# Optimization experiments

Measured on AMD Instinct MI355X. Metric: run time of the kernel, lower is better.

Reference implementation:

```python
import jax, jax.numpy as jnp
import numpy as np

N_DST = 100000


def setup_inputs() -> dict:
    key = jax.random.key(0)
    ks = jax.random.split(key, 12)
    R, Ns, E, Din, H = 3, 100000, 1000000, 128, 64
    return {
        "dst_feat": jax.random.normal(ks[0], (N_DST, Din), jnp.float32),
        "neigh_feats": jax.random.normal(ks[1], (R, Ns, Din), jnp.float32),
        "Wt": jax.random.normal(ks[2], (R + 1, Din, H), jnp.float32) * 0.05,
        "bt": jnp.zeros((R + 1, H), jnp.float32),
        "attn_l": jax.random.normal(ks[3], (R, H), jnp.float32) * 0.1,
        "attn_r": jax.random.normal(ks[4], (R, H), jnp.float32) * 0.1,
        "W1": jax.random.normal(ks[5], (H, 128), jnp.float32) * 0.1,
        "b1": jnp.zeros((128,), jnp.float32),
        "w2": jax.random.normal(ks[6], (128, 1), jnp.float32) * 0.1,
        "src_idx": jax.random.randint(ks[7], (R, E), 0, Ns, jnp.int32),
        "dst_idx": jax.random.randint(ks[8], (R, E), 0, N_DST, jnp.int32),
    }


def _gat_relation(h_src, h_dst, al, ar, src, dst):
    # el/er: per-node attention logits (dot with attn vectors)
    el = h_src @ al  # [Ns]
    er = h_dst @ ar  # [Nd]
    e = jax.nn.leaky_relu(el[src] + er[dst], 0.01)  # [E]
    # edge softmax per destination node (segment softmax)
    m = jax.ops.segment_max(e, dst, num_segments=N_DST)
    a = jnp.exp(e - m[dst])
    s = jax.ops.segment_sum(a, dst, num_segments=N_DST)
    a = a / s[dst]
    # weighted aggregation: sum_e a_e * h_src[src_e]
    out = jax.ops.segment_sum(h_src[src] * a[:, None], dst, num_segments=N_DST)
    return jax.nn.elu(out)


def reference(dst_feat, neigh_feats, Wt, bt, attn_l, attn_r, W1, b1, w2, src_idx, dst_idx):
    R = neigh_feats.shape[0]
    h_dst = dst_feat @ Wt[0] + bt[0]  # weight_T[0]
    z_r = []
    for r in range(R):
        h_src = neigh_feats[r] @ Wt[r + 1] + bt[r + 1]
        z_r.append(_gat_relation(h_src, h_dst, attn_l[r], attn_r[r], src_idx[r], dst_idx[r]))
    z_r = jnp.stack(z_r, axis=1)  # [N, R, D]
    # semantic attention
    w = (jnp.tanh(z_r @ W1 + b1) @ w2).mean(axis=0)  # [R, 1]
    a_w = jax.nn.softmax(w, axis=0)  # softmax over relations
    z = (z_r * a_w[None]).sum(axis=1)  # [N, D]
    return z
```

## Files before the change

### kernel.cpp

```cpp
#include <hip/hip_runtime.h>
#include <hip/hip_fp16.h>

#define N_DST 100000
#define DIN 128
#define HDIM 64
#define RREL 3
#define NE 1000000

#define NBKT_REL 196
#define NBKT (RREL * NBKT_REL)
#define NSEG (RREL * N_DST)
#define EDGE_CHUNK 16384
#define NBLK_BIN ((RREL * NE + EDGE_CHUNK - 1) / EDGE_CHUNK)

typedef _Float16 f16x8 __attribute__((ext_vector_type(8)));
typedef float f32x4 __attribute__((ext_vector_type(4)));

__global__ __launch_bounds__(256) void k_gemm(
    const float* __restrict__ dst_feat, const float* __restrict__ neigh,
    const float* __restrict__ Wt, const float* __restrict__ bt,
    const float* __restrict__ attn_l, const float* __restrict__ attn_r,
    __half* __restrict__ h16, float* __restrict__ el, float* __restrict__ er) {
  const int RB = (N_DST + 127) / 128;
  int mat = blockIdx.x / RB;
  int row0 = (blockIdx.x % RB) * 128;
  const float* A = (mat == 0) ? dst_feat : (neigh + (size_t)(mat - 1) * N_DST * DIN);
  const float* W = Wt + (size_t)mat * DIN * HDIM;
  const float* b = bt + mat * HDIM;

  __shared__ __align__(16) unsigned char lds[48 * 1024];
  unsigned char* ldsA = lds;
  unsigned char* ldsW = lds + 32768;

  int tid = threadIdx.x;

#pragma unroll
  for (int i = 0; i < 8; i++) {
    int s = tid + 256 * i;
    int row = s >> 4;
    int kb = s & 15;
    int gr = row0 + row;
    if (gr >= N_DST) gr = N_DST - 1;
    const float* ap = A + (size_t)gr * DIN + kb * 8;
    float4 v0 = *(const float4*)ap;
    float4 v1 = *(const float4*)(ap + 4);
    f16x8 hv;
    hv[0] = (_Float16)v0.x; hv[1] = (_Float16)v0.y;
    hv[2] = (_Float16)v0.z; hv[3] = (_Float16)v0.w;
    hv[4] = (_Float16)v1.x; hv[5] = (_Float16)v1.y;
    hv[6] = (_Float16)v1.z; hv[7] = (_Float16)v1.w;
    *(f16x8*)(ldsA + row * 256 + ((kb * 16) ^ ((row & 7) << 4))) = hv;
  }

  {
    int col = tid & 63;
    int kq = tid >> 6;
    const float* wp = W + (size_t)(kq * 32) * HDIM + col;
    float wr[32];
#pragma unroll
    for (int m = 0; m < 32; m++) wr[m] = wp[(size_t)m * HDIM];
#pragma unroll
    for (int m8 = 0; m8 < 4; m8++) {
      f16x8 hv;
#pragma unroll
      for (int j = 0; j < 8; j++) hv[j] = (_Float16)wr[m8 * 8 + j];
      int byt = kq * 64 + m8 * 16;
      *(f16x8*)(ldsW + col * 256 + (byt ^ ((col & 7) << 4))) = hv;
    }
  }
  __syncthreads();

  int w = tid >> 6;
  int l = tid & 63;
  int li = l & 15;
  int hi = l >> 4;
  f32x4 acc[2][4] = {};
#pragma unroll
  for (int ks = 0; ks < 4; ks++) {
    int kbyte = ks * 64 + hi * 16;
    f16x8 af[2], bf[4];
#pragma unroll
    for (int rt = 0; rt < 2; rt++) {
      int row = w * 32 + rt * 16 + li;
      af[rt] = *(f16x8*)(ldsA + row * 256 + (kbyte ^ ((row & 7) << 4)));
    }
#pragma unroll
    for (int ct = 0; ct < 4; ct++) {
      int col = ct * 16 + li;
      bf[ct] = *(f16x8*)(ldsW + col * 256 + (kbyte ^ ((col & 7) << 4)));
    }
#pragma unroll
    for (int rt = 0; rt < 2; rt++)
#pragma unroll
      for (int ct = 0; ct < 4; ct++)
        acc[rt][ct] = __builtin_amdgcn_mfma_f32_16x16x32_f16(af[rt], bf[ct], acc[rt][ct], 0, 0, 0);
  }

  float bv[4];
#pragma unroll
  for (int ct = 0; ct < 4; ct++) bv[ct] = b[ct * 16 + li];
#pragma unroll
  for (int rt = 0; rt < 2; rt++)
#pragma unroll
    for (int ct = 0; ct < 4; ct++)
#pragma unroll
      for (int j = 0; j < 4; j++) acc[rt][ct][j] += bv[ct];

  if (mat == 0) {
#pragma unroll
    for (int r = 0; r < RREL; r++) {
      float av[4];
#pragma unroll
      for (int ct = 0; ct < 4; ct++) av[ct] = attn_r[r * HDIM + ct * 16 + li];
#pragma unroll
      for (int rt = 0; rt < 2; rt++) {
        float p[4];
#pragma unroll
        for (int j = 0; j < 4; j++)
          p[j] = acc[rt][0][j] * av[0] + acc[rt][1][j] * av[1] +
                 acc[rt][2][j] * av[2] + acc[rt][3][j] * av[3];
#pragma unroll
        for (int o = 1; o < 16; o <<= 1)
#pragma unroll
          for (int j = 0; j < 4; j++) p[j] += __shfl_xor(p[j], o);
        if (li == 0) {
#pragma unroll
          for (int j = 0; j < 4; j++) {
            int gr = row0 + w * 32 + rt * 16 + hi * 4 + j;
            if (gr < N_DST) er[r * N_DST + gr] = p[j];
          }
        }
      }
    }
  } else {
    int r = mat - 1;
    float av[4];
#pragma unroll
    for (int ct = 0; ct < 4; ct++) av[ct] = attn_l[r * HDIM + ct * 16 + li];
#pragma unroll
    for (int rt = 0; rt < 2; rt++) {
      float p[4];
#pragma unroll
      for (int j = 0; j < 4; j++)
        p[j] = acc[rt][0][j] * av[0] + acc[rt][1][j] * av[1] +
               acc[rt][2][j] * av[2] + acc[rt][3][j] * av[3];
#pragma unroll
      for (int o = 1; o < 16; o <<= 1)
#pragma unroll
        for (int j = 0; j < 4; j++) p[j] += __shfl_xor(p[j], o);
      if (li == 0) {
#pragma unroll
        for (int j = 0; j < 4; j++) {
          int gr = row0 + w * 32 + rt * 16 + hi * 4 + j;
          if (gr < N_DST) el[r * N_DST + gr] = p[j];
        }
      }
    }
    __half* hb = h16 + (size_t)r * N_DST * HDIM;
#pragma unroll
    for (int rt = 0; rt < 2; rt++)
#pragma unroll
      for (int j = 0; j < 4; j++) {
        int gr = row0 + w * 32 + rt * 16 + hi * 4 + j;
        if (gr < N_DST) {
#pragma unroll
          for (int ct = 0; ct < 4; ct++)
            hb[(size_t)gr * HDIM + ct * 16 + li] = __float2half(acc[rt][ct][j]);
        }
      }
  }
}


__global__ __launch_bounds__(256) void k_hist(const int* __restrict__ dst_idx,
                                              int* __restrict__ hist) {
  __shared__ int h[NBKT];
  int tid = threadIdx.x;
  int blk = blockIdx.x;
  for (int i = tid; i < NBKT; i += 256) h[i] = 0;
  __syncthreads();
  int e0 = blk * EDGE_CHUNK;
  int e1 = min(e0 + EDGE_CHUNK, RREL * NE);
  for (int idx = e0 + tid; idx < e1; idx += 256) {
    int r = idx / NE;
    int d = dst_idx[idx];
    atomicAdd(&h[r * NBKT_REL + (d >> 9)], 1);
  }
  __syncthreads();
  for (int i = tid; i < NBKT; i += 256)
    hist[(size_t)i * NBLK_BIN + blk] = h[i];
}

__global__ __launch_bounds__(256) void k_colscan(int* __restrict__ hist,
                                                 int* __restrict__ bcounts) {
  __shared__ int sm[256];
  int b = blockIdx.x;
  int tid = threadIdx.x;
  int v = (tid < NBLK_BIN) ? hist[(size_t)b * NBLK_BIN + tid] : 0;
  sm[tid] = v;
  __syncthreads();
  for (int off = 1; off < 256; off <<= 1) {
    int t = (tid >= off) ? sm[tid - off] : 0;
    __syncthreads();
    sm[tid] += t;
    __syncthreads();
  }
  if (tid < NBLK_BIN) hist[(size_t)b * NBLK_BIN + tid] = sm[tid] - v;
  if (tid == 255) bcounts[b] = sm[255];
}

__global__ __launch_bounds__(256) void k_bscan(const int* __restrict__ bcounts,
                                               int* __restrict__ bucket_base,
                                               int* __restrict__ offsets) {
  __shared__ int sm[256];
  int tid = threadIdx.x;
  int base = tid * 3;
  int c[3];
#pragma unroll
  for (int k = 0; k < 3; k++) c[k] = (base + k < NBKT) ? bcounts[base + k] : 0;
  int tsum = c[0] + c[1] + c[2];
  sm[tid] = tsum;
  __syncthreads();
  for (int off = 1; off < 256; off <<= 1) {
    int v = (tid >= off) ? sm[tid - off] : 0;
    __syncthreads();
    sm[tid] += v;
    __syncthreads();
  }
  int run = sm[tid] - tsum;
#pragma unroll
  for (int k = 0; k < 3; k++) {
    if (base + k < NBKT) bucket_base[base + k] = run;
    run += c[k];
  }
  if (tid == 255) bucket_base[NBKT] = sm[255];
  if (tid == 0) offsets[NSEG] = RREL * NE;
}

__global__ __launch_bounds__(256) void k_place(const int* __restrict__ src_idx,
                                               const int* __restrict__ dst_idx,
                                               const int* __restrict__ hist,
                                               const int* __restrict__ bucket_base,
                                               unsigned* __restrict__ tmp) {
  __shared__ int cur[NBKT];
  int tid = threadIdx.x;
  int blk = blockIdx.x;
  for (int i = tid; i < NBKT; i += 256)
    cur[i] = bucket_base[i] + hist[(size_t)i * NBLK_BIN + blk];
  __syncthreads();
  int e0 = blk * EDGE_CHUNK;
  int e1 = min(e0 + EDGE_CHUNK, RREL * NE);
  for (int idx = e0 + tid; idx < e1; idx += 256) {
    int r = idx / NE;
    int d = dst_idx[idx];
    int s = src_idx[idx];
    int bucket = r * NBKT_REL + (d >> 9);
    int pos = atomicAdd(&cur[bucket], 1);
    tmp[pos] = ((unsigned)(d & 511) << 17) | (unsigned)s;
  }
}

__global__ __launch_bounds__(256) void k_bucket_csr(
    const int* __restrict__ bucket_base, const unsigned* __restrict__ tmp,
    int* __restrict__ src_sorted, int* __restrict__ offsets) {
  __shared__ int cnt[512];
  __shared__ int base_l[512];
  __shared__ int sm[256];
  int b = blockIdx.x;
  int r = b / NBKT_REL;
  int brel = b - r * NBKT_REL;
  int gbase = bucket_base[b];
  int gend = bucket_base[b + 1];
  int tid = threadIdx.x;
  cnt[tid] = 0;
  cnt[tid + 256] = 0;
  __syncthreads();
  for (int e = gbase + tid; e < gend; e += 256)
    atomicAdd(&cnt[tmp[e] >> 17], 1);
  __syncthreads();
  int c0 = cnt[2 * tid], c1 = cnt[2 * tid + 1];
  int tsum = c0 + c1;
  sm[tid] = tsum;
  __syncthreads();
  for (int off = 1; off < 256; off <<= 1) {
    int v = (tid >= off) ? sm[tid - off] : 0;
    __syncthreads();
    sm[tid] += v;
    __syncthreads();
  }
  int run = sm[tid] - tsum;
  base_l[2 * tid] = run;
  base_l[2 * tid + 1] = run + c0;
  __syncthreads();
  for (int s = tid; s < 512; s += 256) {
    int dst = (brel << 9) + s;
    if (dst < N_DST) offsets[r * N_DST + dst] = gbase + base_l[s];
    cnt[s] = 0;
  }
  __syncthreads();
  for (int e = gbase + tid; e < gend; e += 256) {
    unsigned w = tmp[e];
    int s = w >> 17;
    int pos = gbase + base_l[s] + atomicAdd(&cnt[s], 1);
    src_sorted[pos] = (int)(w & 0x1FFFFu);
  }
}

__global__ __launch_bounds__(256) void k_aggregate(
    const int* __restrict__ offsets, const int* __restrict__ src_sorted,
    const float* __restrict__ el, const float* __restrict__ er,
    const __half* __restrict__ h16, float* __restrict__ zbuf) {
  int gw = (blockIdx.x * 256 + threadIdx.x) >> 6;
  int lane = threadIdx.x & 63;
  if (gw >= RREL * N_DST) return;
  int r = gw / N_DST;
  int start = offsets[gw], end = offsets[gw + 1];
  float erv = er[gw];
  const __half* hs = h16 + (size_t)r * N_DST * HDIM;
  const float* elr = el + (size_t)r * N_DST;
  int g = lane >> 4;
  int li = lane & 15;
  float ax = 0.f, ay = 0.f, az = 0.f, aw = 0.f;
  float ssum = 0.f;
  for (int base = start; base < end; base += 64) {
    int cnt = end - base;
    if (cnt > 64) cnt = 64;
    float a = 0.f;
    int sidx = 0;
    if (lane < cnt) {
      sidx = src_sorted[base + lane];
      float x = elr[sidx] + erv;
      x = (x > 0.f) ? x : 0.01f * x;
      a = __expf(x);
    }
    ssum += a;
    int iters = (cnt + 3) >> 2;
    for (int i = 0; i < iters; i++) {
      int j = 4 * i + g;
      float aj = __shfl(a, j);
      int sj = __shfl(sidx, j);
      if (j < cnt) {
        float2 rv = *(const float2*)(hs + ((size_t)sj << 6) + 4 * li);
        float2 lo = __half22float2(*(const __half2*)&rv.x);
        float2 hi = __half22float2(*(const __half2*)&rv.y);
        ax += aj * lo.x;
        ay += aj * lo.y;
        az += aj * hi.x;
        aw += aj * hi.y;
      }
    }
  }
#pragma unroll
  for (int o = 32; o > 0; o >>= 1) ssum += __shfl_xor(ssum, o);
#pragma unroll
  for (int o = 16; o <= 32; o <<= 1) {
    ax += __shfl_xor(ax, o);
    ay += __shfl_xor(ay, o);
    az += __shfl_xor(az, o);
    aw += __shfl_xor(aw, o);
  }
  if (g == 0) {
    float4 zv = make_float4(0.f, 0.f, 0.f, 0.f);
    if (end > start) {
      float inv = 1.f / ssum;
      float v;
      v = ax * inv; zv.x = (v > 0.f) ? v : (__expf(v) - 1.f);
      v = ay * inv; zv.y = (v > 0.f) ? v : (__expf(v) - 1.f);
      v = az * inv; zv.z = (v > 0.f) ? v : (__expf(v) - 1.f);
      v = aw * inv; zv.w = (v > 0.f) ? v : (__expf(v) - 1.f);
    }
    *(float4*)(zbuf + (size_t)gw * HDIM + 4 * li) = zv;
  }
}

__global__ __launch_bounds__(256) void k_semantic(
    const float* __restrict__ zbuf, const float* __restrict__ W1,
    const float* __restrict__ b1, const float* __restrict__ w2,
    float* __restrict__ w_acc) {
  __shared__ float W1l[64 * 128];
  __shared__ float zsh[64 * 68];
  __shared__ float wsum[RREL];
  int tid = threadIdx.x;
  if (tid < RREL) wsum[tid] = 0.f;
  for (int i = tid * 4; i < 64 * 128; i += 1024)
    *(float4*)(W1l + i) = *(const float4*)(W1 + i);
  long row0 = (long)blockIdx.x * 64;
  for (int t4 = tid; t4 < 1024; t4 += 256) {
    int rl = t4 >> 4;
    int j4 = (t4 & 15) << 2;
    long row = row0 + rl;
    float4 v = make_float4(0.f, 0.f, 0.f, 0.f);
    if (row < (long)NSEG) v = *(const float4*)(zbuf + row * HDIM + j4);
    *(float4*)(zsh + rl * 68 + j4) = v;
  }
  __syncthreads();
  int tc = tid & 31;
  int tr = tid >> 5;
  float acc[8][4] = {};
#pragma unroll 1
  for (int jj = 0; jj < 64; jj += 4) {
    float4 wv[4];
#pragma unroll
    for (int j = 0; j < 4; j++) wv[j] = *(float4*)(W1l + (jj + j) * 128 + 4 * tc);
#pragma unroll
    for (int ih = 0; ih < 2; ih++) {
      float4 zv[4];
#pragma unroll
      for (int i = 0; i < 4; i++) zv[i] = *(float4*)(zsh + (8 * tr + 4 * ih + i) * 68 + jj);
#pragma unroll
      for (int i = 0; i < 4; i++) {
        const float* zp = (const float*)&zv[i];
#pragma unroll
        for (int j = 0; j < 4; j++) {
          const float* wp = (const float*)&wv[j];
          float zz = zp[j];
#pragma unroll
          for (int c = 0; c < 4; c++) acc[4 * ih + i][c] += zz * wp[c];
        }
      }
    }
  }
  float b1v[4], w2v[4];
#pragma unroll
  for (int c = 0; c < 4; c++) {
    b1v[c] = b1[4 * tc + c];
    w2v[c] = w2[4 * tc + c];
  }
#pragma unroll
  for (int i = 0; i < 8; i++) {
    long row = row0 + 8 * tr + i;
    float p = 0.f;
#pragma unroll
    for (int c = 0; c < 4; c++) {
      float x = acc[i][c] + b1v[c];
      float ex = __expf(2.f * x);
      p += (1.f - 2.f / (ex + 1.f)) * w2v[c];
    }
#pragma unroll
    for (int o = 16; o > 0; o >>= 1) p += __shfl_xor(p, o);
    if (tc == 0 && row < (long)NSEG) {
      int r = (int)(row / N_DST);
      atomicAdd(&wsum[r], p);
    }
  }
  __syncthreads();
  if (tid < RREL) atomicAdd(&w_acc[tid], wsum[tid]);
}

__global__ __launch_bounds__(256) void k_final(const float* __restrict__ zbuf,
                                               const float* __restrict__ w_acc,
                                               float* __restrict__ out) {
  int idx = blockIdx.x * 256 + threadIdx.x;
  if (idx >= N_DST * HDIM / 4) return;
  const float invN = 1.0f / N_DST;
  float w0 = w_acc[0] * invN, w1 = w_acc[1] * invN, w2v = w_acc[2] * invN;
  float m = fmaxf(w0, fmaxf(w1, w2v));
  float e0 = __expf(w0 - m), e1 = __expf(w1 - m), e2 = __expf(w2v - m);
  float inv = 1.f / (e0 + e1 + e2);
  e0 *= inv; e1 *= inv; e2 *= inv;
  size_t o = (size_t)idx * 4;
  const size_t stride = (size_t)N_DST * HDIM;
  float4 z0 = *(const float4*)(zbuf + o);
  float4 z1 = *(const float4*)(zbuf + stride + o);
  float4 z2 = *(const float4*)(zbuf + 2 * stride + o);
  float4 r;
  r.x = e0 * z0.x + e1 * z1.x + e2 * z2.x;
  r.y = e0 * z0.y + e1 * z1.y + e2 * z2.y;
  r.z = e0 * z0.z + e1 * z1.z + e2 * z2.z;
  r.w = e0 * z0.w + e1 * z1.w + e2 * z2.w;
  *(float4*)(out + o) = r;
}

extern "C" void kernel_launch(void* const* d_in, const int* in_sizes, int n_in,
                              void* d_out, int out_size, void* d_ws, size_t ws_size,
                              hipStream_t stream) {
  const float* dst_feat = (const float*)d_in[0];
  const float* neigh = (const float*)d_in[1];
  const float* Wt = (const float*)d_in[2];
  const float* bt = (const float*)d_in[3];
  const float* attn_l = (const float*)d_in[4];
  const float* attn_r = (const float*)d_in[5];
  const float* W1 = (const float*)d_in[6];
  const float* b1 = (const float*)d_in[7];
  const float* w2 = (const float*)d_in[8];
  const int* src_idx = (const int*)d_in[9];
  const int* dst_idx = (const int*)d_in[10];
  float* out = (float*)d_out;

  char* p = (char*)d_ws;
  auto alloc = [&](size_t bytes) {
    char* q = p;
    p += (bytes + 255) & ~(size_t)255;
    return (void*)q;
  };
  __half* h16 = (__half*)alloc((size_t)RREL * N_DST * HDIM * 2);
  float* el = (float*)alloc((size_t)RREL * N_DST * 4);
  float* er = (float*)alloc((size_t)RREL * N_DST * 4);
  float* zbuf = (float*)alloc((size_t)RREL * N_DST * HDIM * 4);
  float* w_acc = (float*)alloc(64);
  int* offsets = (int*)alloc(((size_t)NSEG + 1) * 4);
  int* hist = (int*)alloc((size_t)NBKT * NBLK_BIN * 4);
  int* bcounts = (int*)alloc((size_t)NBKT * 4);
  int* bucket_base = (int*)alloc((size_t)(NBKT + 1) * 4);
  unsigned* tmp = (unsigned*)alloc((size_t)RREL * NE * 4);
  int* src_sorted = (int*)alloc((size_t)RREL * NE * 4);

  hipMemsetAsync(w_acc, 0, 64, stream);

  k_gemm<<<4 * ((N_DST + 127) / 128), 256, 0, stream>>>(dst_feat, neigh, Wt, bt, attn_l, attn_r,
                                                        h16, el, er);
  k_hist<<<NBLK_BIN, 256, 0, stream>>>(dst_idx, hist);
  k_colscan<<<NBKT, 256, 0, stream>>>(hist, bcounts);
  k_bscan<<<1, 256, 0, stream>>>(bcounts, bucket_base, offsets);
  k_place<<<NBLK_BIN, 256, 0, stream>>>(src_idx, dst_idx, hist, bucket_base, tmp);
  k_bucket_csr<<<NBKT, 256, 0, stream>>>(bucket_base, tmp, src_sorted, offsets);
  k_aggregate<<<(RREL * N_DST * 64) / 256, 256, 0, stream>>>(offsets, src_sorted, el, er, h16, zbuf);
  k_semantic<<<(NSEG + 63) / 64, 256, 0, stream>>>(zbuf, W1, b1, w2, w_acc);
  k_final<<<(N_DST * HDIM / 4 + 255) / 256, 256, 0, stream>>>(zbuf, w_acc, out);
}
```

Baseline: 608.0 us.

## Aggregate each destination with 8 lanes instead of a full wavefront

The segment aggregation now assigns 8 threads to each destination node instead of a 64-lane wavefront. Each thread loads 16 bytes (8 halves) of the source row and walks the edges serially with a one-ahead prefetch of the next source index, so the shuffle broadcasts and cross-lane reductions go away. With an average of about 10 edges per node, the old layout left most lanes idle. The new layout uses lanes better and packs 8 nodes per wavefront, at the cost of serial edge loops and load imbalance between nodes with different degrees.

```diff
diff --git a/kernel.cpp b/kernel.cpp
--- a/kernel.cpp
+++ b/kernel.cpp
@@ -310,67 +310,43 @@
     const int* __restrict__ offsets, const int* __restrict__ src_sorted,
     const float* __restrict__ el, const float* __restrict__ er,
     const __half* __restrict__ h16, float* __restrict__ zbuf) {
-  int gw = (blockIdx.x * 256 + threadIdx.x) >> 6;
-  int lane = threadIdx.x & 63;
-  if (gw >= RREL * N_DST) return;
+  int gw = blockIdx.x * 32 + (threadIdx.x >> 3);
+  int li = threadIdx.x & 7;
+  if (gw >= NSEG) return;
   int r = gw / N_DST;
   int start = offsets[gw], end = offsets[gw + 1];
   float erv = er[gw];
-  const __half* hs = h16 + (size_t)r * N_DST * HDIM;
+  const unsigned char* hs = (const unsigned char*)(h16 + (size_t)r * N_DST * HDIM);
   const float* elr = el + (size_t)r * N_DST;
-  int g = lane >> 4;
-  int li = lane & 15;
-  float ax = 0.f, ay = 0.f, az = 0.f, aw = 0.f;
+  float acc[8] = {};
   float ssum = 0.f;
-  for (int base = start; base < end; base += 64) {
-    int cnt = end - base;
-    if (cnt > 64) cnt = 64;
-    float a = 0.f;
-    int sidx = 0;
-    if (lane < cnt) {
-      sidx = src_sorted[base + lane];
-      float x = elr[sidx] + erv;
-      x = (x > 0.f) ? x : 0.01f * x;
-      a = __expf(x);
-    }
+  int sNext = (start < end) ? src_sorted[start] : 0;
+  for (int e = start; e < end; ++e) {
+    int s = sNext;
+    if (e + 1 < end) sNext = src_sorted[e + 1];
+    float x = elr[s] + erv;
+    float4 rv = *(const float4*)(hs + (unsigned)(s * 128 + li * 16));
+    x = (x > 0.f) ? x : 0.01f * x;
+    float a = __expf(x);
     ssum += a;
-    int iters = (cnt + 3) >> 2;
-    for (int i = 0; i < iters; i++) {
-      int j = 4 * i + g;
-      float aj = __shfl(a, j);
-      int sj = __shfl(sidx, j);
-      if (j < cnt) {
-        float2 rv = *(const float2*)(hs + ((size_t)sj << 6) + 4 * li);
-        float2 lo = __half22float2(*(const __half2*)&rv.x);
-        float2 hi = __half22float2(*(const __half2*)&rv.y);
-        ax += aj * lo.x;
-        ay += aj * lo.y;
-        az += aj * hi.x;
-        aw += aj * hi.y;
-      }
-    }
-  }
-#pragma unroll
-  for (int o = 32; o > 0; o >>= 1) ssum += __shfl_xor(ssum, o);
-#pragma unroll
-  for (int o = 16; o <= 32; o <<= 1) {
-    ax += __shfl_xor(ax, o);
-    ay += __shfl_xor(ay, o);
-    az += __shfl_xor(az, o);
-    aw += __shfl_xor(aw, o);
-  }
-  if (g == 0) {
-    float4 zv = make_float4(0.f, 0.f, 0.f, 0.f);
-    if (end > start) {
-      float inv = 1.f / ssum;
-      float v;
-      v = ax * inv; zv.x = (v > 0.f) ? v : (__expf(v) - 1.f);
-      v = ay * inv; zv.y = (v > 0.f) ? v : (__expf(v) - 1.f);
-      v = az * inv; zv.z = (v > 0.f) ? v : (__expf(v) - 1.f);
-      v = aw * inv; zv.w = (v > 0.f) ? v : (__expf(v) - 1.f);
-    }
-    *(float4*)(zbuf + (size_t)gw * HDIM + 4 * li) = zv;
-  }
+    const __half2* hp = (const __half2*)&rv;
+#pragma unroll
+    for (int q = 0; q < 4; q++) {
+      float2 f = __half22float2(hp[q]);
+      acc[2 * q] += a * f.x;
+      acc[2 * q + 1] += a * f.y;
+    }
+  }
+  float inv = (end > start) ? 1.f / ssum : 0.f;
+  float zv[8];
+#pragma unroll
+  for (int q = 0; q < 8; q++) {
+    float v = acc[q] * inv;
+    zv[q] = (v > 0.f) ? v : (__expf(v) - 1.f);
+  }
+  float* zp = zbuf + (size_t)gw * HDIM + li * 8;
+  *(float4*)zp = make_float4(zv[0], zv[1], zv[2], zv[3]);
+  *(float4*)(zp + 4) = make_float4(zv[4], zv[5], zv[6], zv[7]);
 }
 
 __global__ __launch_bounds__(256) void k_semantic(
@@ -514,7 +490,7 @@
   k_bscan<<<1, 256, 0, stream>>>(bcounts, bucket_base, offsets);
   k_place<<<NBLK_BIN, 256, 0, stream>>>(src_idx, dst_idx, hist, bucket_base, tmp);
   k_bucket_csr<<<NBKT, 256, 0, stream>>>(bucket_base, tmp, src_sorted, offsets);
-  k_aggregate<<<(RREL * N_DST * 64) / 256, 256, 0, stream>>>(offsets, src_sorted, el, er, h16, zbuf);
+  k_aggregate<<<(NSEG + 31) / 32, 256, 0, stream>>>(offsets, src_sorted, el, er, h16, zbuf);
   k_semantic<<<(NSEG + 63) / 64, 256, 0, stream>>>(zbuf, W1, b1, w2, w_acc);
   k_final<<<(N_DST * HDIM / 4 + 255) / 256, 256, 0, stream>>>(zbuf, w_acc, out);
 }
```

Result: faster. 545.9 us (-10.2%).
